# Kernel tuning notes

Measured on AMD Instinct MI355X. Metric: run time of the kernel, lower is better.

Reference implementation:

```python
import jax, jax.numpy as jnp
import numpy as np

B = 16384      # batch size
NL = 131072    # total labels (~8 per image)
S = 7          # grid size
NCLS = 20


def setup_inputs() -> dict:
    key = jax.random.key(0)
    k1, k2, k3, k4, k5 = jax.random.split(key, 5)
    # predictions in [0,1): slices 24:26 / 28:30 feed sqrt(x+1e-6)
    output = jax.random.uniform(k1, (B, S, S, 30), dtype=jnp.float32)
    bidx = jax.random.randint(k2, (NL,), 0, B).astype(jnp.float32)
    cls = jax.random.randint(k3, (NL,), 0, NCLS).astype(jnp.float32)
    cxy = jax.random.uniform(k4, (NL, 2), minval=0.01, maxval=0.99, dtype=jnp.float32)
    wh = jax.random.uniform(k5, (NL, 2), minval=0.05, maxval=0.5, dtype=jnp.float32)
    labels = jnp.concatenate([bidx[:, None], cls[:, None], cxy, wh], axis=1)
    return {"output": output, "labels": labels}


def _iou(a, g):
    # center-format boxes [n,4] = (cx, cy, w, h), standard IoU
    ax1, ax2 = a[:, 0] - a[:, 2] / 2, a[:, 0] + a[:, 2] / 2
    ay1, ay2 = a[:, 1] - a[:, 3] / 2, a[:, 1] + a[:, 3] / 2
    gx1, gx2 = g[:, 0] - g[:, 2] / 2, g[:, 0] + g[:, 2] / 2
    gy1, gy2 = g[:, 1] - g[:, 3] / 2, g[:, 1] + g[:, 3] / 2
    iw = jnp.maximum(0.0, jnp.minimum(ax2, gx2) - jnp.maximum(ax1, gx1))
    ih = jnp.maximum(0.0, jnp.minimum(ay2, gy2) - jnp.maximum(ay1, gy1))
    inter = iw * ih
    union = a[:, 2] * a[:, 3] + g[:, 2] * g[:, 3] - inter
    return inter / (union + 1e-6)


def reference(output, labels):
    w_coord, w_noobj, eps = 5.0, 0.5, 1e-6
    bsz = output.shape[0]
    # no-object confidence penalty over ALL cells (per-label responsible-box
    # terms subtract their share back below, exactly as the torch loop does)
    noobj_loss = w_noobj * jnp.sum(output[..., 20] ** 2 + output[..., 21] ** 2)

    b = labels[:, 0].astype(jnp.int32)
    c = labels[:, 1].astype(jnp.int32)
    gt = labels[:, 2:6]                       # global (cx, cy, w, h)
    rowf = jnp.floor(gt[:, 0] * S)            # int(cx*7)
    colf = jnp.floor(gt[:, 1] * S)            # int(cy*7)
    row = rowf.astype(jnp.int32)
    col = colf.astype(jnp.int32)

    p = output[b, row, col]                   # [nl, 30] gather of responsible cells

    # classification loss
    onehot = jax.nn.one_hot(c, NCLS, dtype=p.dtype)
    class_loss = jnp.sum((p[:, :NCLS] - onehot) ** 2)

    # predicted boxes in global normalized coords: (row + bx)/7 (img_size cancels)
    def to_global(box):
        return jnp.stack(
            [(rowf + box[:, 0]) / S, (colf + box[:, 1]) / S, box[:, 2], box[:, 3]],
            axis=1,
        )

    iou1 = _iou(to_global(p[:, 22:26]), gt)
    iou2 = _iou(to_global(p[:, 26:30]), gt)
    use1 = iou1 >= iou2

    # gt center relative to its cell: gt*7 - row (img_size cancels)
    gt_cell_xy = jnp.stack([gt[:, 0] * S - rowf, gt[:, 1] * S - colf], axis=1)

    xy = jnp.where(use1[:, None], p[:, 22:24], p[:, 26:28])
    wh = jnp.where(use1[:, None], p[:, 24:26], p[:, 28:30])
    coor_loss = w_coord * (
        jnp.sum((xy - gt_cell_xy) ** 2)
        + jnp.sum((jnp.sqrt(wh + eps) - jnp.sqrt(gt[:, 2:4] + eps)) ** 2)
    )

    conf_pred = jnp.where(use1, p[:, 20], p[:, 21])
    conf_tgt = jnp.where(use1, iou1, iou2)
    conf_loss = noobj_loss + jnp.sum(
        (conf_pred - conf_tgt) ** 2 - w_noobj * conf_pred ** 2
    )

    return (coor_loss + conf_loss + class_loss) / bsz
```

## Files before the change

### kernel.cpp

```cpp
#include <hip/hip_runtime.h>
#include <math.h>

constexpr int   kS      = 7;
constexpr int   kNCls   = 20;
constexpr int   kB      = 16384;
constexpr int   kNCells = kB * kS * kS;
constexpr float kWCoord = 5.0f;
constexpr float kWNoobj = 0.5f;
constexpr float kEps    = 1e-6f;

constexpr int kBlocks = 2048;
constexpr int kThreads = 256;

__device__ __forceinline__ float block_reduce(float v) {
    #pragma unroll
    for (int off = 32; off > 0; off >>= 1)
        v += __shfl_down(v, off, 64);
    __shared__ float smem[kThreads / 64];
    const int lane = threadIdx.x & 63;
    const int wv   = threadIdx.x >> 6;
    if (lane == 0) smem[wv] = v;
    __syncthreads();
    float t = 0.0f;
    if (threadIdx.x == 0) {
        #pragma unroll
        for (int i = 0; i < kThreads / 64; ++i) t += smem[i];
    }
    return t;
}

__device__ __forceinline__ float iou_f(float ax, float ay, float aw, float ah,
                                       float gx, float gy, float gw, float gh) {
    const float ax1 = ax - aw * 0.5f, ax2 = ax + aw * 0.5f;
    const float ay1 = ay - ah * 0.5f, ay2 = ay + ah * 0.5f;
    const float gx1 = gx - gw * 0.5f, gx2 = gx + gw * 0.5f;
    const float gy1 = gy - gh * 0.5f, gy2 = gy + gh * 0.5f;
    const float iw = fmaxf(0.0f, fminf(ax2, gx2) - fmaxf(ax1, gx1));
    const float ih = fmaxf(0.0f, fminf(ay2, gy2) - fmaxf(ay1, gy1));
    const float inter = iw * ih;
    const float uni = aw * ah + gw * gh - inter;
    return inter / (uni + kEps);
}

__global__ void __launch_bounds__(kThreads)
fused_kernel(const float* __restrict__ out,
             const float* __restrict__ labels,
             int nl,
             float* __restrict__ partials) {
    const int tid    = blockIdx.x * blockDim.x + threadIdx.x;
    const int stride = gridDim.x * blockDim.x;
    float sum = 0.0f;

    for (int c = tid; c < kNCells; c += stride) {
        const float2 v = *reinterpret_cast<const float2*>(out + (size_t)c * 30 + 20);
        sum += kWNoobj * (v.x * v.x + v.y * v.y);
    }

    for (int l = tid; l < nl; l += stride) {
        const float2* lab2 = reinterpret_cast<const float2*>(labels + (size_t)l * 6);
        const float2 l0 = lab2[0];
        const float2 l1 = lab2[1];
        const float2 l2 = lab2[2];
        const int   c  = (int)l0.y;
        const float gx = l1.x, gy = l1.y, gw = l2.x, gh = l2.y;

        const float rowf = floorf(gx * (float)kS);
        const float colf = floorf(gy * (float)kS);
        const int row = (int)rowf;
        const int col = (int)colf;
        const int b   = (int)l0.x;

        const float* p = out + ((size_t)b * (kS * kS) + row * kS + col) * 30;
        const float2* p2 = reinterpret_cast<const float2*>(p);
        float pv[30];
        #pragma unroll
        for (int j = 0; j < 15; ++j) {
            const float2 t = p2[j];
            pv[2 * j]     = t.x;
            pv[2 * j + 1] = t.y;
        }

        float cl = 0.0f;
        #pragma unroll
        for (int j = 0; j < kNCls; ++j) {
            const float d = pv[j] - ((j == c) ? 1.0f : 0.0f);
            cl += d * d;
        }

        const float g1x = (rowf + pv[22]) / (float)kS;
        const float g1y = (colf + pv[23]) / (float)kS;
        const float g2x = (rowf + pv[26]) / (float)kS;
        const float g2y = (colf + pv[27]) / (float)kS;

        const float iou1 = iou_f(g1x, g1y, pv[24], pv[25], gx, gy, gw, gh);
        const float iou2 = iou_f(g2x, g2y, pv[28], pv[29], gx, gy, gw, gh);
        const bool use1 = (iou1 >= iou2);

        const float gtx_cell = gx * (float)kS - rowf;
        const float gty_cell = gy * (float)kS - colf;
        const float px = use1 ? pv[22] : pv[26];
        const float py = use1 ? pv[23] : pv[27];
        const float pw = use1 ? pv[24] : pv[28];
        const float ph = use1 ? pv[25] : pv[29];
        const float dx = px - gtx_cell;
        const float dy = py - gty_cell;
        const float dw = sqrtf(pw + kEps) - sqrtf(gw + kEps);
        const float dh = sqrtf(ph + kEps) - sqrtf(gh + kEps);
        const float coord = kWCoord * (dx * dx + dy * dy + dw * dw + dh * dh);

        const float cp = use1 ? pv[20] : pv[21];
        const float ct = use1 ? iou1 : iou2;
        const float conf = (cp - ct) * (cp - ct) - kWNoobj * cp * cp;

        sum += cl + coord + conf;
    }

    const float bsum = block_reduce(sum);
    if (threadIdx.x == 0) partials[blockIdx.x] = bsum;
}

__global__ void __launch_bounds__(kThreads)
finalize_kernel(const float* __restrict__ partials, int n, float* __restrict__ out) {
    float s = 0.0f;
    for (int i = threadIdx.x; i < n; i += blockDim.x) s += partials[i];
    const float t = block_reduce(s);
    if (threadIdx.x == 0) out[0] = t * (1.0f / (float)kB);
}

extern "C" void kernel_launch(void* const* d_in, const int* in_sizes, int n_in,
                              void* d_out, int out_size, void* d_ws, size_t ws_size,
                              hipStream_t stream) {
    const float* output = (const float*)d_in[0];
    const float* labels = (const float*)d_in[1];
    float* out = (float*)d_out;
    float* partials = (float*)d_ws;

    const int nl = in_sizes[1] / 6;

    fused_kernel<<<kBlocks, kThreads, 0, stream>>>(output, labels, nl, partials);
    finalize_kernel<<<1, kThreads, 0, stream>>>(partials, kBlocks, out);
}
```

Before: 146.3 us.

## Replace finalize kernel with atomicAdd and use contiguous label chunks per block

Removes the second finalize launch and the workspace partials. The output is zeroed with a memset and each block atomically adds its scaled partial sum into it. The label loop also changes from a grid-stride pattern to contiguous per-block chunks. This makes float summation order nondeterministic and adds a memset node, in exchange for one fewer kernel launch.

```diff
diff --git a/kernel.cpp b/kernel.cpp
--- a/kernel.cpp
+++ b/kernel.cpp
@@ -9,7 +9,7 @@
 constexpr float kWNoobj = 0.5f;
 constexpr float kEps    = 1e-6f;
 
-constexpr int kBlocks = 2048;
+constexpr int kBlocks  = 2048;
 constexpr int kThreads = 256;
 
 __device__ __forceinline__ float block_reduce(float v) {
@@ -46,7 +46,7 @@
 fused_kernel(const float* __restrict__ out,
              const float* __restrict__ labels,
              int nl,
-             float* __restrict__ partials) {
+             float* __restrict__ result) {
     const int tid    = blockIdx.x * blockDim.x + threadIdx.x;
     const int stride = gridDim.x * blockDim.x;
     float sum = 0.0f;
@@ -56,7 +56,12 @@
         sum += kWNoobj * (v.x * v.x + v.y * v.y);
     }
 
-    for (int l = tid; l < nl; l += stride) {
+    const int lpb  = (nl + gridDim.x - 1) / gridDim.x;
+    const int base = blockIdx.x * lpb;
+    for (int j = threadIdx.x; j < lpb; j += blockDim.x) {
+        const int l = base + j;
+        if (l >= nl) break;
+
         const float2* lab2 = reinterpret_cast<const float2*>(labels + (size_t)l * 6);
         const float2 l0 = lab2[0];
         const float2 l1 = lab2[1];
@@ -74,16 +79,16 @@
         const float2* p2 = reinterpret_cast<const float2*>(p);
         float pv[30];
         #pragma unroll
-        for (int j = 0; j < 15; ++j) {
-            const float2 t = p2[j];
-            pv[2 * j]     = t.x;
-            pv[2 * j + 1] = t.y;
+        for (int j2 = 0; j2 < 15; ++j2) {
+            const float2 t = p2[j2];
+            pv[2 * j2]     = t.x;
+            pv[2 * j2 + 1] = t.y;
         }
 
         float cl = 0.0f;
         #pragma unroll
-        for (int j = 0; j < kNCls; ++j) {
-            const float d = pv[j] - ((j == c) ? 1.0f : 0.0f);
+        for (int j2 = 0; j2 < kNCls; ++j2) {
+            const float d = pv[j2] - ((j2 == c) ? 1.0f : 0.0f);
             cl += d * d;
         }
 
@@ -116,15 +121,8 @@
     }
 
     const float bsum = block_reduce(sum);
-    if (threadIdx.x == 0) partials[blockIdx.x] = bsum;
-}
-
-__global__ void __launch_bounds__(kThreads)
-finalize_kernel(const float* __restrict__ partials, int n, float* __restrict__ out) {
-    float s = 0.0f;
-    for (int i = threadIdx.x; i < n; i += blockDim.x) s += partials[i];
-    const float t = block_reduce(s);
-    if (threadIdx.x == 0) out[0] = t * (1.0f / (float)kB);
+    if (threadIdx.x == 0)
+        atomicAdd(result, bsum * (1.0f / (float)kB));
 }
 
 extern "C" void kernel_launch(void* const* d_in, const int* in_sizes, int n_in,
@@ -133,10 +131,10 @@
     const float* output = (const float*)d_in[0];
     const float* labels = (const float*)d_in[1];
     float* out = (float*)d_out;
-    float* partials = (float*)d_ws;
 
     const int nl = in_sizes[1] / 6;
 
-    fused_kernel<<<kBlocks, kThreads, 0, stream>>>(output, labels, nl, partials);
-    finalize_kernel<<<1, kThreads, 0, stream>>>(partials, kBlocks, out);
+    hipMemsetAsync(out, 0, sizeof(float), stream);
+
+    fused_kernel<<<kBlocks, kThreads, 0, stream>>>(output, labels, nl, out);
 }
```

New measurement: 165.9 us. 13.4% more time.
